# Optimization experiments

Hardware: AMD Instinct MI355X
Metric: run time of the kernel (lower is better)

Reference implementation:

```python
import jax, jax.numpy as jnp
import numpy as np

R, M1, N1, M2, N2 = 4, 1024, 2048, 2, 4
BATCH, SEQ = 4, 2048


def setup_inputs() -> dict:
    key = jax.random.key(0)
    k_x, k_A, k_B, k_b, k_p, k_q = jax.random.split(key, 6)
    x = jax.random.normal(k_x, (BATCH, SEQ, M1 * M2), dtype=jnp.float32)
    A = jax.random.normal(k_A, (R, N1, M1), dtype=jnp.float32) * 0.001
    B = jax.random.normal(k_B, (R, M2, N2), dtype=jnp.float32) * 0.001
    b = jnp.zeros((N1 * N2,), dtype=jnp.float32)
    p_inv = jax.random.permutation(k_p, M1 * M2).astype(jnp.int32)
    q = jax.random.permutation(k_q, N1 * N2).astype(jnp.int32)
    return {"x": x, "A": A, "B": B, "b": b, "p_inv": p_inv, "q": q}


def reference(x, A, B, b, p_inv, q):
    # x: [Bt, S, m1*m2]; A: [r, n1, m1]; B: [r, m2, n2]
    r, n1, m1 = A.shape
    _, m2, n2 = B.shape
    shape = x.shape
    tokens = shape[0] * shape[1]
    # input permutation gather (use_p=True)
    xp = x[:, :, p_inv]
    # Bx = einsum('km,rmn->rkn'): [r, tokens*m1, n2]
    xf = xp.reshape(-1, m2)
    Bx = jnp.einsum('km,rmn->rkn', xf, B)
    Bx = Bx.reshape(r, tokens, m1, n2)
    # ABx = einsum('rnm,rbmj->bnj'): [tokens, n1, n2]
    ABx = jnp.einsum('rnm,rbmj->bnj', A, Bx)
    ABx = ABx.reshape(shape[:-1] + (n1 * n2,))
    # output permutation gather (use_q=True) + bias
    out = ABx[:, :, q] + b
    return out
```

## Files before the change

kernel.cpp:

```cpp
#include <hip/hip_runtime.h>
#include <hip/hip_bf16.h>

typedef unsigned short u16;
typedef __attribute__((ext_vector_type(8))) short short8;
typedef __attribute__((ext_vector_type(4))) float floatx4;

#define TOKENS 8192
#define KDIM   2048
#define NFEAT  8192
#define R_     4
#define N1_    2048
#define M1_    1024

#define BM 256
#define BN 256
#define BK 64
#define NITER (KDIM / (2 * BK))

__device__ __forceinline__ u16 f2bf(float f) {
  union { float f; unsigned u; } v; v.f = f;
  unsigned r = v.u + 0x7fffu + ((v.u >> 16) & 1u);
  return (u16)(r >> 16);
}

#define CVT_BLOCKS 16384
struct u16x4 { u16 a, b, c, d; };
__global__ void k_prep(const float4* __restrict__ x4, u16x4* __restrict__ xb,
                       const float* __restrict__ A, const float* __restrict__ Bm,
                       const int* __restrict__ p_inv, const int* __restrict__ q,
                       u16* __restrict__ Wf) {
  __shared__ int pfs[KDIM];
  int bid = blockIdx.x;
  if (bid < CVT_BLOCKS) {
    int i = bid * 256 + threadIdx.x;
    float4 v = x4[i];
    u16x4 o; o.a = f2bf(v.x); o.b = f2bf(v.y); o.c = f2bf(v.z); o.d = f2bf(v.w);
    xb[i] = o;
  } else {
    int f = bid - CVT_BLOCKS;
    for (int i = threadIdx.x; i < KDIM; i += 256) pfs[p_inv[i]] = i;
    __syncthreads();
    int k0 = threadIdx.x * 8;
    int qf = q[f];
    int n = qf >> 2, jq = qf & 3;
    const float* An = A + (size_t)n * M1_;
    float bc[8];
#pragma unroll
    for (int r = 0; r < R_; ++r) {
      bc[r * 2 + 0] = Bm[r * 8 + 0 * 4 + jq];
      bc[r * 2 + 1] = Bm[r * 8 + 1 * 4 + jq];
    }
    u16 w[8];
#pragma unroll
    for (int i = 0; i < 8; ++i) {
      int c = pfs[k0 + i];
      int m1 = c >> 1, m2 = c & 1;
      float acc = 0.f;
#pragma unroll
      for (int r = 0; r < R_; ++r)
        acc += An[(size_t)r * (N1_ * M1_) + m1] * bc[r * 2 + m2];
      w[i] = f2bf(acc);
    }
    *(short8*)(Wf + (size_t)f * KDIM + k0) = *(const short8*)w;
  }
}

#define GLD16(gp, lp) __builtin_amdgcn_global_load_lds( \
    (const __attribute__((address_space(1))) void*)(gp), \
    (__attribute__((address_space(3))) void*)(lp), 16, 0, 0)

#define FENCE asm volatile("" ::: "memory")
#define BAR   do { FENCE; __builtin_amdgcn_s_barrier(); FENCE; } while (0)
#define LGKM0 asm volatile("s_waitcnt lgkmcnt(0)" ::: "memory")
#define VMCNT(n) asm volatile("s_waitcnt vmcnt(" #n ")" ::: "memory")

__global__ __launch_bounds__(512, 2) void k_gemm(
    const u16* __restrict__ X, const u16* __restrict__ W,
    const float* __restrict__ bias, float* __restrict__ out) {
  __shared__ __align__(16) char lds[2 * 65536];

  int bid = blockIdx.x;
  int xcd = bid & 7;
  int loc = bid >> 3;
  int u = loc >> 5, v = loc & 31;
  int tM = xcd * 4 + (v >> 3);
  int tN = u * 8 + (v & 7);
  int rowBase = tM * BM, colBase = tN * BN;

  int tid = threadIdx.x, lane = tid & 63, wave = tid >> 6;
  int wm = wave >> 2;
  int wn = wave & 3;

  int srow = tid >> 3;
  int scol = ((tid & 7) ^ (srow & 7)) * 8;
  const u16* Asrc = X + (size_t)(rowBase + srow) * KDIM + scol;
  const u16* Bsrc = W + (size_t)(colBase + srow) * KDIM + scol;

  auto SA = [&](int slot, int half, int kt) {
#pragma unroll
    for (int jj = 0; jj < 2; ++jj)
      GLD16(Asrc + (size_t)(half * 128 + jj * 64) * KDIM + kt * 64,
            &lds[slot * 65536 + half * 16384 + jj * 8192 + tid * 16]);
  };
  auto SB = [&](int slot, int half, int kt) {
#pragma unroll
    for (int jj = 0; jj < 2; ++jj)
      GLD16(Bsrc + (size_t)(half * 128 + jj * 64) * KDIM + kt * 64,
            &lds[slot * 65536 + 32768 + half * 16384 + jj * 8192 + tid * 16]);
  };

  int l15 = lane & 15, lhi = lane >> 4, l7 = lane & 7;
  int x0 = (lhi ^ l7) * 16;
  int x1 = ((4 + lhi) ^ l7) * 16;
  int abase = wm * 16384 + l15 * 128;
  int bbase = 32768 + (wn >> 1) * 16384 + ((wn & 1) * 64 + l15) * 128;

  auto RA = [&](int slot, int m, int kk) -> short8 {
    return *(const short8*)&lds[slot * 65536 + abase + m * 2048 + (kk ? x1 : x0)];
  };
  auto RB = [&](int slot, int n, int kk) -> short8 {
    return *(const short8*)&lds[slot * 65536 + bbase + n * 2048 + (kk ? x1 : x0)];
  };

  floatx4 acc[8][4] = {};
  short8 a[4][2], a2[4][2], b[2][2], b2[2][2];

  auto RDa = [&](int slot) {
#pragma unroll
    for (int m = 0; m < 4; ++m) { a[m][0] = RA(slot, m, 0); a[m][1] = RA(slot, m, 1); }
  };
  auto RDa2 = [&](int slot) {
#pragma unroll
    for (int m = 0; m < 4; ++m) { a2[m][0] = RA(slot, 4 + m, 0); a2[m][1] = RA(slot, 4 + m, 1); }
  };
  auto RDb = [&](int slot) {
#pragma unroll
    for (int n = 0; n < 2; ++n) { b[n][0] = RB(slot, n, 0); b[n][1] = RB(slot, n, 1); }
  };
  auto RDb2 = [&](int slot) {
#pragma unroll
    for (int n = 0; n < 2; ++n) { b2[n][0] = RB(slot, 2 + n, 0); b2[n][1] = RB(slot, 2 + n, 1); }
  };

  auto MM = [&](short8 (&Af)[4][2], short8 (&Bf)[2][2], int mo, int no) {
    __builtin_amdgcn_s_setprio(1);
#pragma unroll
    for (int m = 0; m < 4; ++m)
#pragma unroll
      for (int n = 0; n < 2; ++n) {
        acc[mo + m][no + n] = __builtin_amdgcn_mfma_f32_16x16x32_bf16(Af[m][0], Bf[n][0], acc[mo + m][no + n], 0, 0, 0);
        acc[mo + m][no + n] = __builtin_amdgcn_mfma_f32_16x16x32_bf16(Af[m][1], Bf[n][1], acc[mo + m][no + n], 0, 0, 0);
      }
    __builtin_amdgcn_s_setprio(0);
  };

  SA(0, 0, 0); SA(0, 1, 0); SB(0, 0, 0); SB(0, 1, 0);
  SA(1, 0, 1); SA(1, 1, 1); SB(1, 0, 1); SB(1, 1, 1);
  VMCNT(8);
  BAR;
  RDa(0); RDb(0);

  for (int it = 0; it < NITER - 1; ++it) {
    int t0 = 2 * it;
    LGKM0; RDa2(0);
    MM(a, b, 0, 0);
    FENCE;
    LGKM0; RDb2(0);
    MM(a2, b, 4, 0);
    BAR;
    LGKM0;
    SA(0, 0, t0 + 2); SA(0, 1, t0 + 2);
    MM(a2, b2, 4, 2);
    VMCNT(4);
    BAR;
    LGKM0;
    SB(0, 0, t0 + 2); SB(0, 1, t0 + 2);
    MM(a, b2, 0, 2);
    RDa(1); RDb(1);
    FENCE;
    LGKM0; RDa2(1);
    MM(a, b, 0, 0);
    FENCE;
    LGKM0; RDb2(1);
    MM(a2, b, 4, 0);
    BAR;
    LGKM0;
    SA(1, 0, t0 + 3); SA(1, 1, t0 + 3);
    MM(a2, b2, 4, 2);
    VMCNT(4);
    BAR;
    LGKM0;
    SB(1, 0, t0 + 3); SB(1, 1, t0 + 3);
    MM(a, b2, 0, 2);
    RDa(0); RDb(0);
    FENCE;
  }

  {
    LGKM0; RDa2(0); MM(a, b, 0, 0); FENCE;
    LGKM0; RDb2(0); MM(a2, b, 4, 0); BAR;
    LGKM0; MM(a2, b2, 4, 2); VMCNT(0); BAR;
    LGKM0; MM(a, b2, 0, 2); RDa(1); RDb(1); FENCE;
    LGKM0; RDa2(1); MM(a, b, 0, 0); FENCE;
    LGKM0; RDb2(1); MM(a2, b, 4, 0); FENCE;
    LGKM0; MM(a2, b2, 4, 2); FENCE;
    LGKM0; MM(a, b2, 0, 2);
  }

  float bv[4];
#pragma unroll
  for (int n = 0; n < 4; ++n)
    bv[n] = bias[colBase + wn * 64 + n * 16 + l15];
#pragma unroll
  for (int m = 0; m < 8; ++m) {
    int r0 = wm * 128 + m * 16 + (lhi << 2);
#pragma unroll
    for (int n = 0; n < 4; ++n) {
      size_t basep = (size_t)(rowBase + r0) * NFEAT + colBase + wn * 64 + n * 16 + l15;
#pragma unroll
      for (int reg = 0; reg < 4; ++reg)
        out[basep + (size_t)reg * NFEAT] = acc[m][n][reg] + bv[n];
    }
  }
}

extern "C" void kernel_launch(void* const* d_in, const int* in_sizes, int n_in,
                              void* d_out, int out_size, void* d_ws, size_t ws_size,
                              hipStream_t stream) {
  const float* x     = (const float*)d_in[0];
  const float* A     = (const float*)d_in[1];
  const float* Bm    = (const float*)d_in[2];
  const float* bias  = (const float*)d_in[3];
  const int*   p_inv = (const int*)d_in[4];
  const int*   q     = (const int*)d_in[5];
  float* out = (float*)d_out;

  u16* Xb = (u16*)d_ws;
  u16* Wf = (u16*)((char*)d_ws + (size_t)TOKENS * KDIM * 2);

  k_prep<<<CVT_BLOCKS + NFEAT, 256, 0, stream>>>((const float4*)x, (u16x4*)Xb, A, Bm, p_inv, q, Wf);
  k_gemm<<<(TOKENS / BM) * (NFEAT / BN), 512, 0, stream>>>(Xb, Wf, bias, out);
}
```

Baseline: 307.0 us.

## Replace hand-interleaved GEMM main loop with simple double-buffered phase pipeline

The finely interleaved main loop, with its partial-fragment register double buffering, explicit lgkmcnt waits and half-tile staged global-to-LDS loads, is replaced by a simpler per-k-tile phase. Each phase issues all async loads for the next tile into the other LDS slot, then reads the full A/B fragments for the current tile and runs all MFMAs, and finally waits on vmcnt(0) and a barrier. This reduces the number of barriers and scheduling complexity and lets the compiler schedule LDS reads. The trade-off is less fine-grained overlap between LDS reads and MFMAs, a full vmcnt(0) stall each tile, and higher register pressure from holding 12 fragments at once.

```diff
diff --git a/kernel.cpp b/kernel.cpp
--- a/kernel.cpp
+++ b/kernel.cpp
@@ -15,7 +15,7 @@
 #define BM 256
 #define BN 256
 #define BK 64
-#define NITER (KDIM / (2 * BK))
+#define NKT (KDIM / BK)
 
 __device__ __forceinline__ u16 f2bf(float f) {
   union { float f; unsigned u; } v; v.f = f;
@@ -71,7 +71,6 @@
 
 #define FENCE asm volatile("" ::: "memory")
 #define BAR   do { FENCE; __builtin_amdgcn_s_barrier(); FENCE; } while (0)
-#define LGKM0 asm volatile("s_waitcnt lgkmcnt(0)" ::: "memory")
 #define VMCNT(n) asm volatile("s_waitcnt vmcnt(" #n ")" ::: "memory")
 
 __global__ __launch_bounds__(512, 2) void k_gemm(
@@ -123,88 +122,45 @@
   };
 
   floatx4 acc[8][4] = {};
-  short8 a[4][2], a2[4][2], b[2][2], b2[2][2];
 
-  auto RDa = [&](int slot) {
+  auto PHASE = [&](int cs, int t, bool full) {
+    if (full) {
+      SA(cs ^ 1, 0, t + 1); SA(cs ^ 1, 1, t + 1);
+      SB(cs ^ 1, 0, t + 1); SB(cs ^ 1, 1, t + 1);
+    }
+    short8 af[8], bf[4];
 #pragma unroll
-    for (int m = 0; m < 4; ++m) { a[m][0] = RA(slot, m, 0); a[m][1] = RA(slot, m, 1); }
-  };
-  auto RDa2 = [&](int slot) {
+    for (int m = 0; m < 8; ++m) af[m] = RA(cs, m, 0);
 #pragma unroll
-    for (int m = 0; m < 4; ++m) { a2[m][0] = RA(slot, 4 + m, 0); a2[m][1] = RA(slot, 4 + m, 1); }
-  };
-  auto RDb = [&](int slot) {
-#pragma unroll
-    for (int n = 0; n < 2; ++n) { b[n][0] = RB(slot, n, 0); b[n][1] = RB(slot, n, 1); }
-  };
-  auto RDb2 = [&](int slot) {
-#pragma unroll
-    for (int n = 0; n < 2; ++n) { b2[n][0] = RB(slot, 2 + n, 0); b2[n][1] = RB(slot, 2 + n, 1); }
-  };
-
-  auto MM = [&](short8 (&Af)[4][2], short8 (&Bf)[2][2], int mo, int no) {
+    for (int n = 0; n < 4; ++n) bf[n] = RB(cs, n, 0);
     __builtin_amdgcn_s_setprio(1);
 #pragma unroll
-    for (int m = 0; m < 4; ++m)
+    for (int m = 0; m < 8; ++m)
 #pragma unroll
-      for (int n = 0; n < 2; ++n) {
-        acc[mo + m][no + n] = __builtin_amdgcn_mfma_f32_16x16x32_bf16(Af[m][0], Bf[n][0], acc[mo + m][no + n], 0, 0, 0);
-        acc[mo + m][no + n] = __builtin_amdgcn_mfma_f32_16x16x32_bf16(Af[m][1], Bf[n][1], acc[mo + m][no + n], 0, 0, 0);
-      }
+      for (int n = 0; n < 4; ++n)
+        acc[m][n] = __builtin_amdgcn_mfma_f32_16x16x32_bf16(af[m], bf[n], acc[m][n], 0, 0, 0);
     __builtin_amdgcn_s_setprio(0);
+#pragma unroll
+    for (int m = 0; m < 8; ++m) af[m] = RA(cs, m, 1);
+#pragma unroll
+    for (int n = 0; n < 4; ++n) bf[n] = RB(cs, n, 1);
+    __builtin_amdgcn_s_setprio(1);
+#pragma unroll
+    for (int m = 0; m < 8; ++m)
+#pragma unroll
+      for (int n = 0; n < 4; ++n)
+        acc[m][n] = __builtin_amdgcn_mfma_f32_16x16x32_bf16(af[m], bf[n], acc[m][n], 0, 0, 0);
+    __builtin_amdgcn_s_setprio(0);
+    if (full) { VMCNT(0); BAR; }
   };
 
   SA(0, 0, 0); SA(0, 1, 0); SB(0, 0, 0); SB(0, 1, 0);
-  SA(1, 0, 1); SA(1, 1, 1); SB(1, 0, 1); SB(1, 1, 1);
-  VMCNT(8);
-  BAR;
-  RDa(0); RDb(0);
+  VMCNT(0); BAR;
 
-  for (int it = 0; it < NITER - 1; ++it) {
-    int t0 = 2 * it;
-    LGKM0; RDa2(0);
-    MM(a, b, 0, 0);
-    FENCE;
-    LGKM0; RDb2(0);
-    MM(a2, b, 4, 0);
-    BAR;
-    LGKM0;
-    SA(0, 0, t0 + 2); SA(0, 1, t0 + 2);
-    MM(a2, b2, 4, 2);
-    VMCNT(4);
-    BAR;
-    LGKM0;
-    SB(0, 0, t0 + 2); SB(0, 1, t0 + 2);
-    MM(a, b2, 0, 2);
-    RDa(1); RDb(1);
-    FENCE;
-    LGKM0; RDa2(1);
-    MM(a, b, 0, 0);
-    FENCE;
-    LGKM0; RDb2(1);
-    MM(a2, b, 4, 0);
-    BAR;
-    LGKM0;
-    SA(1, 0, t0 + 3); SA(1, 1, t0 + 3);
-    MM(a2, b2, 4, 2);
-    VMCNT(4);
-    BAR;
-    LGKM0;
-    SB(1, 0, t0 + 3); SB(1, 1, t0 + 3);
-    MM(a, b2, 0, 2);
-    RDa(0); RDb(0);
-    FENCE;
-  }
-
-  {
-    LGKM0; RDa2(0); MM(a, b, 0, 0); FENCE;
-    LGKM0; RDb2(0); MM(a2, b, 4, 0); BAR;
-    LGKM0; MM(a2, b2, 4, 2); VMCNT(0); BAR;
-    LGKM0; MM(a, b2, 0, 2); RDa(1); RDb(1); FENCE;
-    LGKM0; RDa2(1); MM(a, b, 0, 0); FENCE;
-    LGKM0; RDb2(1); MM(a2, b, 4, 0); FENCE;
-    LGKM0; MM(a2, b2, 4, 2); FENCE;
-    LGKM0; MM(a, b2, 0, 2);
+#pragma unroll 1
+  for (int it = 0; it < NKT / 2; ++it) {
+    PHASE(0, 2 * it, true);
+    PHASE(1, 2 * it + 1, 2 * it + 1 < NKT - 1);
   }
 
   float bv[4];
```

After: 327.5 us. 6.7% more time.

## Apply input permutation to activations and remap GEMM tile-to-XCD assignment

Applied to the files above, without the earlier changes.

The p_inv permutation now gathers x during the bf16 conversion, one block per token row. The weight build therefore reads A contiguously with float4 loads and no longer needs the shared-memory inverse-permutation table or its barrier. The GEMM tile mapping also swaps which dimension is grouped per XCD, aiming for better L2 reuse of the weight panel. The trade-off is that the x conversion becomes a scattered gather of 4-byte elements instead of coalesced float4 loads, which could cost bandwidth on the largest input.

```diff
diff --git a/kernel.cpp b/kernel.cpp
--- a/kernel.cpp
+++ b/kernel.cpp
@@ -23,24 +23,23 @@
   return (u16)(r >> 16);
 }
 
-#define CVT_BLOCKS 16384
-struct u16x4 { u16 a, b, c, d; };
-__global__ void k_prep(const float4* __restrict__ x4, u16x4* __restrict__ xb,
+__global__ void k_prep(const float* __restrict__ x, u16* __restrict__ xb,
                        const float* __restrict__ A, const float* __restrict__ Bm,
                        const int* __restrict__ p_inv, const int* __restrict__ q,
                        u16* __restrict__ Wf) {
-  __shared__ int pfs[KDIM];
   int bid = blockIdx.x;
-  if (bid < CVT_BLOCKS) {
-    int i = bid * 256 + threadIdx.x;
-    float4 v = x4[i];
-    u16x4 o; o.a = f2bf(v.x); o.b = f2bf(v.y); o.c = f2bf(v.z); o.d = f2bf(v.w);
-    xb[i] = o;
+  int c0 = threadIdx.x * 8;
+  if (bid < TOKENS) {
+    const float* xrow = x + (size_t)bid * KDIM;
+    int4 i0 = *(const int4*)(p_inv + c0);
+    int4 i1 = *(const int4*)(p_inv + c0 + 4);
+    int idx[8] = {i0.x, i0.y, i0.z, i0.w, i1.x, i1.y, i1.z, i1.w};
+    u16 w[8];
+#pragma unroll
+    for (int i = 0; i < 8; ++i) w[i] = f2bf(xrow[idx[i]]);
+    *(short8*)(xb + (size_t)bid * KDIM + c0) = *(const short8*)w;
   } else {
-    int f = bid - CVT_BLOCKS;
-    for (int i = threadIdx.x; i < KDIM; i += 256) pfs[p_inv[i]] = i;
-    __syncthreads();
-    int k0 = threadIdx.x * 8;
+    int f = bid - TOKENS;
     int qf = q[f];
     int n = qf >> 2, jq = qf & 3;
     const float* An = A + (size_t)n * M1_;
@@ -50,18 +49,21 @@
       bc[r * 2 + 0] = Bm[r * 8 + 0 * 4 + jq];
       bc[r * 2 + 1] = Bm[r * 8 + 1 * 4 + jq];
     }
+    float4 a4[4];
+#pragma unroll
+    for (int r = 0; r < R_; ++r)
+      a4[r] = *(const float4*)(An + (size_t)r * (N1_ * M1_) + (c0 >> 1));
     u16 w[8];
 #pragma unroll
     for (int i = 0; i < 8; ++i) {
-      int c = pfs[k0 + i];
-      int m1 = c >> 1, m2 = c & 1;
+      int mo = i >> 1, m2 = i & 1;
       float acc = 0.f;
 #pragma unroll
       for (int r = 0; r < R_; ++r)
-        acc += An[(size_t)r * (N1_ * M1_) + m1] * bc[r * 2 + m2];
+        acc += ((const float*)&a4[r])[mo] * bc[r * 2 + m2];
       w[i] = f2bf(acc);
     }
-    *(short8*)(Wf + (size_t)f * KDIM + k0) = *(const short8*)w;
+    *(short8*)(Wf + (size_t)f * KDIM + c0) = *(const short8*)w;
   }
 }
 
@@ -83,8 +85,8 @@
   int xcd = bid & 7;
   int loc = bid >> 3;
   int u = loc >> 5, v = loc & 31;
-  int tM = xcd * 4 + (v >> 3);
-  int tN = u * 8 + (v & 7);
+  int tM = u * 8 + (v >> 2);
+  int tN = xcd * 4 + (v & 3);
   int rowBase = tM * BM, colBase = tN * BN;
 
   int tid = threadIdx.x, lane = tid & 63, wave = tid >> 6;
@@ -238,6 +240,6 @@
   u16* Xb = (u16*)d_ws;
   u16* Wf = (u16*)((char*)d_ws + (size_t)TOKENS * KDIM * 2);
 
-  k_prep<<<CVT_BLOCKS + NFEAT, 256, 0, stream>>>((const float4*)x, (u16x4*)Xb, A, Bm, p_inv, q, Wf);
+  k_prep<<<TOKENS + NFEAT, 256, 0, stream>>>(x, Xb, A, Bm, p_inv, q, Wf);
   k_gemm<<<(TOKENS / BM) * (NFEAT / BN), 512, 0, stream>>>(Xb, Wf, bias, out);
 }
```

After: 267.7 us, median of 3. -12.8%, faster.
